# Performance work log

Measured on AMD Instinct MI355X. Metric: run time of the kernel, lower is better.

## Reference

```python
import jax, jax.numpy as jnp
import numpy as np

N_UP, N_DOWN, N_NUC, B = 16, 16, 8, 2048
EMB, TPS = 256, 32
N_ELEC = N_UP + N_DOWN


def mlp(x, w1, b1, w2, b2):
    # subnet: one hidden layer (tanh), linear output
    return jnp.tanh(x @ w1 + b1) @ w2 + b2


def _edge_indices():
    up = np.arange(N_UP)
    down = np.arange(N_UP, N_ELEC)

    def block_pairs(b):
        s, r = np.meshgrid(b, b, indexing='ij')
        m = s != r
        return s[m], r[m]

    s1, r1 = block_pairs(up)
    s2, r2 = block_pairs(down)
    senders_same = np.concatenate([s1, s2])
    receivers_same = np.concatenate([r1, r2])
    su, rd = np.meshgrid(up, down, indexing='ij')
    sd, ru = np.meshgrid(down, up, indexing='ij')
    senders_anti = np.concatenate([su.ravel(), sd.ravel()])
    receivers_anti = np.concatenate([rd.ravel(), ru.ravel()])
    senders_ne = np.repeat(np.arange(N_NUC), N_ELEC)
    receivers_ne = np.tile(np.arange(N_ELEC), N_NUC)
    return (senders_same, receivers_same, senders_anti, receivers_anti,
            senders_ne, receivers_ne)


def setup_inputs() -> dict:
    key = jax.random.key(0)
    ks = iter(jax.random.split(key, 32))

    def p(shape):
        return jax.random.normal(next(ks), shape, jnp.float32) * 0.1

    ss, rs, sa, ra, sn, rn = _edge_indices()
    inp = dict(
        electrons=p((B, N_ELEC, EMB)),
        nuclei=p((B, N_NUC, EMB)),
        feat_same=p((B, len(ss), TPS)),
        feat_anti=p((B, len(sa), TPS)),
        feat_ne=p((B, len(sn), TPS)),
        # u: per-edge-type deep-feature MLPs (TPS -> TPS)
        u_w1=p((3, TPS, TPS)), u_b1=jnp.zeros((3, TPS)),
        u_w2=p((3, TPS, TPS)), u_b2=jnp.zeros((3, TPS)),
        # w: per-edge-type message weight MLPs (TPS -> TPS)
        w_w1=p((3, TPS, TPS)), w_b1=jnp.zeros((3, TPS)),
        w_w2=p((3, TPS, TPS)), w_b2=jnp.zeros((3, TPS)),
        # h: per-edge-type sender-node MLPs (EMB -> TPS)
        h_w1=p((3, EMB, TPS)), h_b1=jnp.zeros((3, TPS)),
        h_w2=p((3, TPS, TPS)), h_b2=jnp.zeros((3, TPS)),
        # g: node update MLP (EMB + 3*TPS -> EMB), update_rule='concatenate'
        g_w1=p((EMB + 3 * TPS, EMB)), g_b1=jnp.zeros((EMB,)),
        g_w2=p((EMB, EMB)), g_b2=jnp.zeros((EMB,)),
        senders_same=jnp.asarray(ss, jnp.int32),
        receivers_same=jnp.asarray(rs, jnp.int32),
        senders_anti=jnp.asarray(sa, jnp.int32),
        receivers_anti=jnp.asarray(ra, jnp.int32),
        senders_ne=jnp.asarray(sn, jnp.int32),
        receivers_ne=jnp.asarray(rn, jnp.int32),
    )
    return inp


def reference(electrons, nuclei, feat_same, feat_anti, feat_ne,
              u_w1, u_b1, u_w2, u_b2,
              w_w1, w_b1, w_w2, w_b2,
              h_w1, h_b1, h_w2, h_b2,
              g_w1, g_b1, g_w2, g_b2,
              senders_same, receivers_same,
              senders_anti, receivers_anti,
              senders_ne, receivers_ne):
    feats = [feat_same, feat_anti, feat_ne]
    senders = [senders_same, senders_anti, senders_ne]
    receivers = [receivers_same, receivers_anti, receivers_ne]
    sender_nodes = [electrons, electrons, nuclei]
    z = []
    for t in range(3):  # fixed small set of edge types: same, anti, ne
        # deep features with two-particle residual (residual add)
        e = feats[t] + mlp(feats[t], u_w1[t], u_b1[t], u_w2[t], u_b2[t])
        we = mlp(e, w_w1[t], w_b1[t], w_w2[t], w_b2[t])              # [B, E_t, TPS]
        hx_nodes = mlp(sender_nodes[t], h_w1[t], h_b1[t], h_w2[t], h_b2[t])
        hx = hx_nodes[:, senders[t]]                                  # gather senders
        msg = we * hx
        # segment-sum over receivers into electron nodes
        zt = jnp.zeros((electrons.shape[0], N_ELEC, msg.shape[-1]), msg.dtype)
        z.append(zt.at[:, receivers[t]].add(msg))
    z_same, z_anti, z_ne = z
    # mean aggregation denominators (self_interaction=False -> self_mod=1)
    den_same = jnp.clip(jnp.concatenate(
        [jnp.full((N_UP, 1), N_UP - 1.0), jnp.full((N_DOWN, 1), N_DOWN - 1.0)]), 1.0)
    den_anti = jnp.clip(jnp.concatenate(
        [jnp.full((N_UP, 1), float(N_DOWN)), jnp.full((N_DOWN, 1), float(N_UP))]), 1.0)
    f = jnp.concatenate(
        [electrons, z_ne / N_NUC, z_same / den_same, z_anti / den_anti], axis=-1)
    updated = mlp(f, g_w1, g_b1, g_w2, g_b2)
    # one-particle residual (add)
    return electrons + updated
```

## Files before the change

### kernel.cpp

```cpp
#include <hip/hip_runtime.h>
#include <math.h>

#define NE 32
#define NN 8
#define EMB 256
#define TPS 32
#define E_SAME 480
#define E_ANTI 512
#define E_NE 256

#define AU1_OFF 0
#define AU2_OFF 3072
#define AW1_OFF 6144
#define AW2_OFF 9216
#define H1T_OFF 12288
#define H2T_OFF 36864
#define BIAS_OFF 39936
#define G1_OFF 40512
#define G2_OFF 130624

typedef float f32x4 __attribute__((ext_vector_type(4)));
typedef short s16x4 __attribute__((ext_vector_type(4)));
typedef short s16x8 __attribute__((ext_vector_type(8)));

__device__ __forceinline__ short f2bf(float x) {
    unsigned u = __builtin_bit_cast(unsigned, x);
    u += 0x7fffu + ((u >> 16) & 1u);
    return (short)(u >> 16);
}
__device__ __forceinline__ float bf2f(short h) {
    unsigned u = ((unsigned)(unsigned short)h) << 16;
    return __builtin_bit_cast(float, u);
}
__device__ __forceinline__ float fast_tanh(float x) {
    float e = __builtin_amdgcn_exp2f(x * 2.8853900817779268f);
    return 1.f - 2.f * __builtin_amdgcn_rcpf(e + 1.f);
}
__device__ __forceinline__ s16x8 pack8(float4 a, float4 b) {
    s16x8 r = { f2bf(a.x), f2bf(a.y), f2bf(a.z), f2bf(a.w),
                f2bf(b.x), f2bf(b.y), f2bf(b.z), f2bf(b.w) };
    return r;
}
__device__ __forceinline__ f32x4 mfma32(s16x8 a, s16x8 b, f32x4 c) {
    return __builtin_amdgcn_mfma_f32_16x16x32_bf16(a, b, c, 0, 0, 0);
}
__device__ __forceinline__ f32x4 mfma16(s16x4 a, s16x4 b, f32x4 c) {
#if __has_builtin(__builtin_amdgcn_mfma_f32_16x16x16bf16_1k)
    return __builtin_amdgcn_mfma_f32_16x16x16bf16_1k(a, b, c, 0, 0, 0);
#else
    asm volatile("v_mfma_f32_16x16x16_bf16 %0, %1, %2, %0" : "+v"(c) : "v"(a), "v"(b));
    return c;
#endif
}

__global__ void prep_weights(const float* __restrict__ u_w1, const float* __restrict__ u_w2,
                             const float* __restrict__ w_w1, const float* __restrict__ w_w2,
                             const float* __restrict__ h_w1, const float* __restrict__ h_w2,
                             const float* __restrict__ u_b1, const float* __restrict__ u_b2,
                             const float* __restrict__ w_b1, const float* __restrict__ w_b2,
                             const float* __restrict__ h_b1, const float* __restrict__ h_b2,
                             const float* __restrict__ g_w1, const float* __restrict__ g_w2,
                             short* __restrict__ wsb)
{
    int tile = blockIdx.x, lane = threadIdx.x;
    int g = lane >> 4, q = lane & 15;
    if (tile < 6) {
        int t = tile >> 1, mt = tile & 1;
        const float* src = u_w1 + t * 1024;
        short* dst = wsb + AU1_OFF + tile * 512 + lane * 8;
        #pragma unroll
        for (int i = 0; i < 8; ++i) dst[i] = f2bf(src[(8 * g + i) * 32 + mt * 16 + q]);
    } else if (tile < 42) {
        int m = (tile - 6) / 12, idx = (tile - 6) % 12;
        int mt = (idx >> 1) & 1, ks = idx & 1, t = idx >> 2;
        const float* mp = (m == 0) ? u_w2 : (m == 1) ? w_w1 : w_w2;
        const float* src = mp + t * 1024;
        short* dst = wsb + AU2_OFF + m * 3072 + idx * 256 + lane * 4;
        #pragma unroll
        for (int i = 0; i < 4; ++i) dst[i] = f2bf(src[(ks * 16 + 4 * g + i) * 32 + mt * 16 + q]);
    } else if (tile < 90) {
        int idx = tile - 42;
        int t = idx >> 4, r = idx & 15, mt = r >> 3, ks = r & 7;
        const float* src = h_w1 + t * 8192;
        short* dst = wsb + H1T_OFF + idx * 512 + lane * 8;
        #pragma unroll
        for (int i = 0; i < 8; ++i) dst[i] = f2bf(src[(ks * 32 + 8 * g + i) * 32 + mt * 16 + q]);
    } else if (tile < 102) {
        int idx = tile - 90;
        int t = idx >> 2, mt = (idx >> 1) & 1, ks = idx & 1;
        const float* src = h_w2 + t * 1024;
        short* dst = wsb + H2T_OFF + idx * 256 + lane * 4;
        #pragma unroll
        for (int i = 0; i < 4; ++i) dst[i] = f2bf(src[(ks * 16 + 4 * g + i) * 32 + mt * 16 + q]);
    } else if (tile == 102) {
        const float* bsrc[6] = {u_b1, u_b2, w_b1, w_b2, h_b1, h_b2};
        for (int j = lane; j < 576; j += 64)
            wsb[BIAS_OFF + j] = f2bf(bsrc[j / 96][j % 96]);
    } else if (tile < 279) {
        int idx = tile - 103, nt = idx / 11, ks = idx % 11;
        short* dst = wsb + G1_OFF + idx * 512 + lane * 8;
        #pragma unroll
        for (int i = 0; i < 8; ++i)
            dst[i] = f2bf(g_w1[(size_t)(ks * 32 + 8 * g + i) * 256 + nt * 16 + q]);
    } else {
        int idx = tile - 279;
        short* dst = wsb + G2_OFF + idx * 512 + lane * 8;
        int nt = idx >> 3, ks = idx & 7;
        #pragma unroll
        for (int i = 0; i < 8; ++i)
            dst[i] = f2bf(g_w2[(size_t)(ks * 32 + 8 * g + i) * 256 + nt * 16 + q]);
    }
}

__launch_bounds__(256, 4)
__global__ void gnn_kernel(
    const float* __restrict__ elec, const float* __restrict__ nuc,
    const float* __restrict__ fs,  const float* __restrict__ fa,  const float* __restrict__ fn,
    const float* __restrict__ g_b1, const float* __restrict__ g_b2,
    const int* __restrict__ ss, const int* __restrict__ rs,
    const int* __restrict__ sa, const int* __restrict__ ra,
    const int* __restrict__ sn, const int* __restrict__ rn,
    const short* __restrict__ wsb,
    float* __restrict__ out)
{
    __shared__ __align__(16) char smem[40384];
    short* f_s  = (short*)smem;
    float* z_s  = (float*)(smem + 22784);
    short* hx_s = (short*)(smem + 35200);
    short* H_s  = (short*)(smem + 22784);

    const int tid  = threadIdx.x;
    const int b    = blockIdx.x;
    const int lane = tid & 63, wv = tid >> 6;
    const int g    = lane >> 4, q = lane & 15;

    if (wv > 0)
        for (int i = tid - 64; i < 32 * 97; i += 192) z_s[i] = 0.f;

    #pragma unroll 1
    for (int task = wv; task < 5; task += 4) {
        int t, nt;
        if (task < 4) { t = task >> 1; nt = task & 1; }
        else          { t = 2; nt = 0; }
        const float* rowp = (t < 2) ? elec + ((size_t)b * NE + nt * 16 + q) * EMB
                                    : nuc  + ((size_t)b * NN + (q < 8 ? q : 7)) * EMB;
        f32x4 c0 = {0.f, 0.f, 0.f, 0.f}, c1 = {0.f, 0.f, 0.f, 0.f};
        const short* wA = wsb + H1T_OFF + t * 16 * 512;
        #pragma unroll
        for (int ks = 0; ks < 8; ++ks) {
            float4 v0 = *(const float4*)(rowp + 32 * ks + 8 * g);
            float4 v1 = *(const float4*)(rowp + 32 * ks + 8 * g + 4);
            s16x8 Bf = pack8(v0, v1);
            if (t == 0) {
                int off = (nt * 16 + q) * 356 + 32 * ks + 8 * g;
                *(s16x4*)(f_s + off)     = __builtin_shufflevector(Bf, Bf, 0, 1, 2, 3);
                *(s16x4*)(f_s + off + 4) = __builtin_shufflevector(Bf, Bf, 4, 5, 6, 7);
            }
            s16x8 a0 = *(const s16x8*)(wA + ks * 512 + lane * 8);
            s16x8 a1 = *(const s16x8*)(wA + (8 + ks) * 512 + lane * 8);
            c0 = mfma32(a0, Bf, c0);
            c1 = mfma32(a1, Bf, c1);
        }
        s16x4 b1l = *(const s16x4*)(wsb + BIAS_OFF + (12 + t) * 32 + 4 * g);
        s16x4 b1h = *(const s16x4*)(wsb + BIAS_OFF + (12 + t) * 32 + 16 + 4 * g);
        s16x4 p0, p1;
        #pragma unroll
        for (int r = 0; r < 4; ++r) {
            p0[r] = f2bf(fast_tanh(c0[r] + bf2f(b1l[r])));
            p1[r] = f2bf(fast_tanh(c1[r] + bf2f(b1h[r])));
        }
        const short* wA2 = wsb + H2T_OFF + t * 4 * 256;
        f32x4 d0 = {0.f, 0.f, 0.f, 0.f}, d1 = {0.f, 0.f, 0.f, 0.f};
        d0 = mfma16(*(const s16x4*)(wA2 + 0 * 256 + lane * 4), p0, d0);
        d0 = mfma16(*(const s16x4*)(wA2 + 1 * 256 + lane * 4), p1, d0);
        d1 = mfma16(*(const s16x4*)(wA2 + 2 * 256 + lane * 4), p0, d1);
        d1 = mfma16(*(const s16x4*)(wA2 + 3 * 256 + lane * 4), p1, d1);
        if (t < 2 || q < 8) {
            s16x4 b2l = *(const s16x4*)(wsb + BIAS_OFF + (15 + t) * 32 + 4 * g);
            s16x4 b2h = *(const s16x4*)(wsb + BIAS_OFF + (15 + t) * 32 + 16 + 4 * g);
            s16x4 w0, w1;
            #pragma unroll
            for (int r = 0; r < 4; ++r) {
                w0[r] = f2bf(d0[r] + bf2f(b2l[r]));
                w1[r] = f2bf(d1[r] + bf2f(b2h[r]));
            }
            int row = t * 32 + nt * 16 + q;
            *(s16x4*)(hx_s + row * 36 + 4 * g)      = w0;
            *(s16x4*)(hx_s + row * 36 + 16 + 4 * g) = w1;
        }
    }
    __syncthreads();

    #pragma unroll 1
    for (int t = 0; t < 3; ++t) {
        const float* ft; const int* snd; const int* rcv; int cnt, zc0;
        if (t == 0)      { ft = fs; snd = ss; rcv = rs; cnt = E_SAME; zc0 = 32; }
        else if (t == 1) { ft = fa; snd = sa; rcv = ra; cnt = E_ANTI; zc0 = 64; }
        else             { ft = fn; snd = sn; rcv = rn; cnt = E_NE;   zc0 = 0;  }
        s16x8 Au1_0 = *(const s16x8*)(wsb + AU1_OFF + (t * 2 + 0) * 512 + lane * 8);
        s16x8 Au1_1 = *(const s16x8*)(wsb + AU1_OFF + (t * 2 + 1) * 512 + lane * 8);
        s16x4 Au2_[4], Aw1_[4], Aw2_[4];
        #pragma unroll
        for (int i = 0; i < 4; ++i) {
            Au2_[i] = *(const s16x4*)(wsb + AU2_OFF + (t * 4 + i) * 256 + lane * 4);
            Aw1_[i] = *(const s16x4*)(wsb + AW1_OFF + (t * 4 + i) * 256 + lane * 4);
            Aw2_[i] = *(const s16x4*)(wsb + AW2_OFF + (t * 4 + i) * 256 + lane * 4);
        }
        s16x4 bb1l = *(const s16x4*)(wsb + BIAS_OFF + (0 + t) * 32 + 4 * g);
        s16x4 bb1h = *(const s16x4*)(wsb + BIAS_OFF + (0 + t) * 32 + 16 + 4 * g);
        s16x4 bb2l = *(const s16x4*)(wsb + BIAS_OFF + (3 + t) * 32 + 4 * g);
        s16x4 bb2h = *(const s16x4*)(wsb + BIAS_OFF + (3 + t) * 32 + 16 + 4 * g);
        s16x4 bb3l = *(const s16x4*)(wsb + BIAS_OFF + (6 + t) * 32 + 4 * g);
        s16x4 bb3h = *(const s16x4*)(wsb + BIAS_OFF + (6 + t) * 32 + 16 + 4 * g);
        s16x4 bb4l = *(const s16x4*)(wsb + BIAS_OFF + (9 + t) * 32 + 4 * g);
        s16x4 bb4h = *(const s16x4*)(wsb + BIAS_OFF + (9 + t) * 32 + 16 + 4 * g);
        const short* hxt = hx_s + t * 32 * 36;
        int ntile = cnt >> 4;

        const float* fp = ft + ((size_t)b * cnt + wv * 16 + q) * TPS;
        float4 v0 = *(const float4*)(fp + 8 * g);
        float4 v1 = *(const float4*)(fp + 8 * g + 4);
        float4 rl = *(const float4*)(fp + 4 * g);
        float4 rh = *(const float4*)(fp + 16 + 4 * g);
        int se = snd[wv * 16 + q], re = rcv[wv * 16 + q];

        #pragma unroll 1
        for (int tt = wv; tt < ntile; tt += 4) {
            int tn = tt + 4;
            float4 n0 = {0,0,0,0}, n1 = {0,0,0,0}, nrl = {0,0,0,0}, nrh = {0,0,0,0};
            int ns = 0, nr = 0;
            if (tn < ntile) {
                const float* np = ft + ((size_t)b * cnt + tn * 16 + q) * TPS;
                n0 = *(const float4*)(np + 8 * g);
                n1 = *(const float4*)(np + 8 * g + 4);
                nrl = *(const float4*)(np + 4 * g);
                nrh = *(const float4*)(np + 16 + 4 * g);
                ns = snd[tn * 16 + q]; nr = rcv[tn * 16 + q];
            }
            s16x8 B32 = pack8(v0, v1);
            f32x4 c0 = {0.f,0.f,0.f,0.f}, c1 = {0.f,0.f,0.f,0.f};
            c0 = mfma32(Au1_0, B32, c0);
            c1 = mfma32(Au1_1, B32, c1);
            s16x4 p0, p1;
            #pragma unroll
            for (int r = 0; r < 4; ++r) {
                p0[r] = f2bf(fast_tanh(c0[r] + bf2f(bb1l[r])));
                p1[r] = f2bf(fast_tanh(c1[r] + bf2f(bb1h[r])));
            }
            f32x4 d0 = {0.f,0.f,0.f,0.f}, d1 = {0.f,0.f,0.f,0.f};
            d0 = mfma16(Au2_[0], p0, d0); d0 = mfma16(Au2_[1], p1, d0);
            d1 = mfma16(Au2_[2], p0, d1); d1 = mfma16(Au2_[3], p1, d1);
            const float* rlp = (const float*)&rl; const float* rhp = (const float*)&rh;
            #pragma unroll
            for (int r = 0; r < 4; ++r) {
                p0[r] = f2bf(rlp[r] + d0[r] + bf2f(bb2l[r]));
                p1[r] = f2bf(rhp[r] + d1[r] + bf2f(bb2h[r]));
            }
            d0 = (f32x4){0.f,0.f,0.f,0.f}; d1 = (f32x4){0.f,0.f,0.f,0.f};
            d0 = mfma16(Aw1_[0], p0, d0); d0 = mfma16(Aw1_[1], p1, d0);
            d1 = mfma16(Aw1_[2], p0, d1); d1 = mfma16(Aw1_[3], p1, d1);
            #pragma unroll
            for (int r = 0; r < 4; ++r) {
                p0[r] = f2bf(fast_tanh(d0[r] + bf2f(bb3l[r])));
                p1[r] = f2bf(fast_tanh(d1[r] + bf2f(bb3h[r])));
            }
            d0 = (f32x4){0.f,0.f,0.f,0.f}; d1 = (f32x4){0.f,0.f,0.f,0.f};
            d0 = mfma16(Aw2_[0], p0, d0); d0 = mfma16(Aw2_[1], p1, d0);
            d1 = mfma16(Aw2_[2], p0, d1); d1 = mfma16(Aw2_[3], p1, d1);
            s16x4 hlo = *(const s16x4*)(hxt + se * 36 + 4 * g);
            s16x4 hhi = *(const s16x4*)(hxt + se * 36 + 16 + 4 * g);
            float* zr = z_s + re * 97 + zc0 + 4 * g;
            #pragma unroll
            for (int r = 0; r < 4; ++r) {
                atomicAdd(zr + r,      (d0[r] + bf2f(bb4l[r])) * bf2f(hlo[r]));
                atomicAdd(zr + 16 + r, (d1[r] + bf2f(bb4h[r])) * bf2f(hhi[r]));
            }
            v0 = n0; v1 = n1; rl = nrl; rh = nrh; se = ns; re = nr;
        }
    }
    __syncthreads();

    for (int i = tid; i < 32 * 96; i += 256) {
        int r = i / 96, c = i - r * 96;
        float sc = (c < 32) ? 0.125f : ((c < 64) ? (1.f / 15.f) : (1.f / 16.f));
        f_s[r * 356 + 256 + c] = f2bf(z_s[r * 97 + c] * sc);
    }
    __syncthreads();

    #pragma unroll 1
    for (int task = wv; task < 32; task += 4) {
        int mt = task >> 4, nt = task & 15;
        f32x4 acc = {0.f, 0.f, 0.f, 0.f};
        const short* ar = f_s + (mt * 16 + q) * 356 + 8 * g;
        const short* wp = wsb + G1_OFF + nt * 11 * 512 + lane * 8;
        #pragma unroll
        for (int ks = 0; ks < 11; ++ks) {
            s16x4 alo = *(const s16x4*)(ar + 32 * ks);
            s16x4 ahi = *(const s16x4*)(ar + 32 * ks + 4);
            s16x8 a = __builtin_shufflevector(alo, ahi, 0, 1, 2, 3, 4, 5, 6, 7);
            s16x8 bw = *(const s16x8*)(wp + ks * 512);
            acc = mfma32(a, bw, acc);
        }
        float bias = g_b1[nt * 16 + q];
        #pragma unroll
        for (int r = 0; r < 4; ++r)
            H_s[(mt * 16 + 4 * g + r) * 260 + nt * 16 + q] = f2bf(fast_tanh(acc[r] + bias));
    }
    __syncthreads();

    #pragma unroll 1
    for (int task = wv; task < 32; task += 4) {
        int mt = task >> 4, nt = task & 15;
        f32x4 acc = {0.f, 0.f, 0.f, 0.f};
        const short* ar = H_s + (mt * 16 + q) * 260 + 8 * g;
        const short* wp = wsb + G2_OFF + nt * 8 * 512 + lane * 8;
        #pragma unroll
        for (int ks = 0; ks < 8; ++ks) {
            s16x4 alo = *(const s16x4*)(ar + 32 * ks);
            s16x4 ahi = *(const s16x4*)(ar + 32 * ks + 4);
            s16x8 a = __builtin_shufflevector(alo, ahi, 0, 1, 2, 3, 4, 5, 6, 7);
            s16x8 bw = *(const s16x8*)(wp + ks * 512);
            acc = mfma32(a, bw, acc);
        }
        float bias = g_b2[nt * 16 + q];
        #pragma unroll
        for (int r = 0; r < 4; ++r) {
            int row = mt * 16 + 4 * g + r, col = nt * 16 + q;
            size_t o = ((size_t)b * NE + row) * EMB + col;
            out[o] = bf2f(f_s[row * 356 + col]) + acc[r] + bias;
        }
    }
}

extern "C" void kernel_launch(void* const* d_in, const int* in_sizes, int n_in,
                              void* d_out, int out_size, void* d_ws, size_t ws_size,
                              hipStream_t stream) {
    const float* elec = (const float*)d_in[0];
    const float* nuc  = (const float*)d_in[1];
    const float* fs   = (const float*)d_in[2];
    const float* fa   = (const float*)d_in[3];
    const float* fn   = (const float*)d_in[4];
    const float* u_w1 = (const float*)d_in[5];
    const float* u_b1 = (const float*)d_in[6];
    const float* u_w2 = (const float*)d_in[7];
    const float* u_b2 = (const float*)d_in[8];
    const float* w_w1 = (const float*)d_in[9];
    const float* w_b1 = (const float*)d_in[10];
    const float* w_w2 = (const float*)d_in[11];
    const float* w_b2 = (const float*)d_in[12];
    const float* h_w1 = (const float*)d_in[13];
    const float* h_b1 = (const float*)d_in[14];
    const float* h_w2 = (const float*)d_in[15];
    const float* h_b2 = (const float*)d_in[16];
    const float* g_w1 = (const float*)d_in[17];
    const float* g_b1 = (const float*)d_in[18];
    const float* g_w2 = (const float*)d_in[19];
    const float* g_b2 = (const float*)d_in[20];
    const int* ss = (const int*)d_in[21];
    const int* rs = (const int*)d_in[22];
    const int* sa = (const int*)d_in[23];
    const int* ra = (const int*)d_in[24];
    const int* sn = (const int*)d_in[25];
    const int* rn = (const int*)d_in[26];

    short* wsb = (short*)d_ws;
    int nb = in_sizes[0] / (NE * EMB);

    prep_weights<<<407, 64, 0, stream>>>(u_w1, u_w2, w_w1, w_w2, h_w1, h_w2,
                                         u_b1, u_b2, w_b1, w_b2, h_b1, h_b2,
                                         g_w1, g_w2, wsb);
    gnn_kernel<<<nb, 256, 0, stream>>>(elec, nuc, fs, fa, fn, g_b1, g_b2,
                                       ss, rs, sa, ra, sn, rn, wsb, (float*)d_out);
}
```

Baseline: 473.6 us.

## Split fused GNN kernel into hx, edge and update kernels via global scratch

Breaks the single per-batch kernel into three launches. One computes sender-node h-MLP outputs for all batches into global memory, one runs the edge MLPs and scatter-add and writes scaled bf16 aggregates to global memory, and one reloads the electrons and aggregates to run the node-update MLP. The aim is to cut per-kernel shared memory and register pressure and to spread the small h-MLP work across all waves instead of leaving three of four waves idle. The cost is extra global round-trips for hx and z, an extra reload of the electrons, and two more kernel launches.

```diff
diff --git a/kernel.cpp b/kernel.cpp
--- a/kernel.cpp
+++ b/kernel.cpp
@@ -18,6 +18,8 @@
 #define BIAS_OFF 39936
 #define G1_OFF 40512
 #define G2_OFF 130624
+#define HX_OFF  196608
+#define ZS_OFF  4915200
 
 typedef float f32x4 __attribute__((ext_vector_type(4)));
 typedef short s16x4 __attribute__((ext_vector_type(4)));
@@ -39,6 +41,11 @@
 __device__ __forceinline__ s16x8 pack8(float4 a, float4 b) {
     s16x8 r = { f2bf(a.x), f2bf(a.y), f2bf(a.z), f2bf(a.w),
                 f2bf(b.x), f2bf(b.y), f2bf(b.z), f2bf(b.w) };
+    return r;
+}
+__device__ __forceinline__ s16x8 pack8v(f32x4 a, f32x4 b) {
+    s16x8 r = { f2bf(a[0]), f2bf(a[1]), f2bf(a[2]), f2bf(a[3]),
+                f2bf(b[0]), f2bf(b[1]), f2bf(b[2]), f2bf(b[3]) };
     return r;
 }
 __device__ __forceinline__ f32x4 mfma32(s16x8 a, s16x8 b, f32x4 c) {
@@ -113,82 +120,77 @@
 }
 
 __launch_bounds__(256, 4)
-__global__ void gnn_kernel(
-    const float* __restrict__ elec, const float* __restrict__ nuc,
+__global__ void hx_kernel(const float* __restrict__ elec, const float* __restrict__ nuc,
+                          const short* __restrict__ wsb, short* __restrict__ hxg)
+{
+    const int lane = threadIdx.x & 63, wv = threadIdx.x >> 6;
+    const int g = lane >> 4, q = lane & 15;
+    const int wave_gid = blockIdx.x * 4 + wv;
+    const int b = wave_gid / 5, task = wave_gid % 5;
+
+    int t, nt;
+    if (task < 4) { t = task >> 1; nt = task & 1; }
+    else          { t = 2; nt = 0; }
+    const float* rowp = (t < 2) ? elec + ((size_t)b * NE + nt * 16 + q) * EMB
+                                : nuc  + ((size_t)b * NN + (q < 8 ? q : 7)) * EMB;
+    f32x4 c0 = {0.f, 0.f, 0.f, 0.f}, c1 = {0.f, 0.f, 0.f, 0.f};
+    const short* wA = wsb + H1T_OFF + t * 16 * 512;
+    #pragma unroll
+    for (int ks = 0; ks < 8; ++ks) {
+        float4 v0 = *(const float4*)(rowp + 32 * ks + 8 * g);
+        float4 v1 = *(const float4*)(rowp + 32 * ks + 8 * g + 4);
+        s16x8 Bf = pack8(v0, v1);
+        s16x8 a0 = *(const s16x8*)(wA + ks * 512 + lane * 8);
+        s16x8 a1 = *(const s16x8*)(wA + (8 + ks) * 512 + lane * 8);
+        c0 = mfma32(a0, Bf, c0);
+        c1 = mfma32(a1, Bf, c1);
+    }
+    s16x4 b1l = *(const s16x4*)(wsb + BIAS_OFF + (12 + t) * 32 + 4 * g);
+    s16x4 b1h = *(const s16x4*)(wsb + BIAS_OFF + (12 + t) * 32 + 16 + 4 * g);
+    s16x4 p0, p1;
+    #pragma unroll
+    for (int r = 0; r < 4; ++r) {
+        p0[r] = f2bf(fast_tanh(c0[r] + bf2f(b1l[r])));
+        p1[r] = f2bf(fast_tanh(c1[r] + bf2f(b1h[r])));
+    }
+    const short* wA2 = wsb + H2T_OFF + t * 4 * 256;
+    f32x4 d0 = {0.f, 0.f, 0.f, 0.f}, d1 = {0.f, 0.f, 0.f, 0.f};
+    d0 = mfma16(*(const s16x4*)(wA2 + 0 * 256 + lane * 4), p0, d0);
+    d0 = mfma16(*(const s16x4*)(wA2 + 1 * 256 + lane * 4), p1, d0);
+    d1 = mfma16(*(const s16x4*)(wA2 + 2 * 256 + lane * 4), p0, d1);
+    d1 = mfma16(*(const s16x4*)(wA2 + 3 * 256 + lane * 4), p1, d1);
+    if (t < 2 || q < 8) {
+        s16x4 b2l = *(const s16x4*)(wsb + BIAS_OFF + (15 + t) * 32 + 4 * g);
+        s16x4 b2h = *(const s16x4*)(wsb + BIAS_OFF + (15 + t) * 32 + 16 + 4 * g);
+        s16x4 w0, w1;
+        #pragma unroll
+        for (int r = 0; r < 4; ++r) {
+            w0[r] = f2bf(d0[r] + bf2f(b2l[r]));
+            w1[r] = f2bf(d1[r] + bf2f(b2h[r]));
+        }
+        int row = t * 32 + nt * 16 + q;
+        short* dst = hxg + ((size_t)b * 72 + row) * 32;
+        *(s16x4*)(dst + 4 * g)      = w0;
+        *(s16x4*)(dst + 16 + 4 * g) = w1;
+    }
+}
+
+__launch_bounds__(256, 4)
+__global__ void edge_kernel(
     const float* __restrict__ fs,  const float* __restrict__ fa,  const float* __restrict__ fn,
-    const float* __restrict__ g_b1, const float* __restrict__ g_b2,
     const int* __restrict__ ss, const int* __restrict__ rs,
     const int* __restrict__ sa, const int* __restrict__ ra,
     const int* __restrict__ sn, const int* __restrict__ rn,
-    const short* __restrict__ wsb,
-    float* __restrict__ out)
+    const short* __restrict__ wsb, const short* __restrict__ hxg,
+    short* __restrict__ zsg)
 {
-    __shared__ __align__(16) char smem[40384];
-    short* f_s  = (short*)smem;
-    float* z_s  = (float*)(smem + 22784);
-    short* hx_s = (short*)(smem + 35200);
-    short* H_s  = (short*)(smem + 22784);
-
+    __shared__ __align__(16) float z_s[32 * 97];
     const int tid  = threadIdx.x;
     const int b    = blockIdx.x;
     const int lane = tid & 63, wv = tid >> 6;
     const int g    = lane >> 4, q = lane & 15;
 
-    if (wv > 0)
-        for (int i = tid - 64; i < 32 * 97; i += 192) z_s[i] = 0.f;
-
-    #pragma unroll 1
-    for (int task = wv; task < 5; task += 4) {
-        int t, nt;
-        if (task < 4) { t = task >> 1; nt = task & 1; }
-        else          { t = 2; nt = 0; }
-        const float* rowp = (t < 2) ? elec + ((size_t)b * NE + nt * 16 + q) * EMB
-                                    : nuc  + ((size_t)b * NN + (q < 8 ? q : 7)) * EMB;
-        f32x4 c0 = {0.f, 0.f, 0.f, 0.f}, c1 = {0.f, 0.f, 0.f, 0.f};
-        const short* wA = wsb + H1T_OFF + t * 16 * 512;
-        #pragma unroll
-        for (int ks = 0; ks < 8; ++ks) {
-            float4 v0 = *(const float4*)(rowp + 32 * ks + 8 * g);
-            float4 v1 = *(const float4*)(rowp + 32 * ks + 8 * g + 4);
-            s16x8 Bf = pack8(v0, v1);
-            if (t == 0) {
-                int off = (nt * 16 + q) * 356 + 32 * ks + 8 * g;
-                *(s16x4*)(f_s + off)     = __builtin_shufflevector(Bf, Bf, 0, 1, 2, 3);
-                *(s16x4*)(f_s + off + 4) = __builtin_shufflevector(Bf, Bf, 4, 5, 6, 7);
-            }
-            s16x8 a0 = *(const s16x8*)(wA + ks * 512 + lane * 8);
-            s16x8 a1 = *(const s16x8*)(wA + (8 + ks) * 512 + lane * 8);
-            c0 = mfma32(a0, Bf, c0);
-            c1 = mfma32(a1, Bf, c1);
-        }
-        s16x4 b1l = *(const s16x4*)(wsb + BIAS_OFF + (12 + t) * 32 + 4 * g);
-        s16x4 b1h = *(const s16x4*)(wsb + BIAS_OFF + (12 + t) * 32 + 16 + 4 * g);
-        s16x4 p0, p1;
-        #pragma unroll
-        for (int r = 0; r < 4; ++r) {
-            p0[r] = f2bf(fast_tanh(c0[r] + bf2f(b1l[r])));
-            p1[r] = f2bf(fast_tanh(c1[r] + bf2f(b1h[r])));
-        }
-        const short* wA2 = wsb + H2T_OFF + t * 4 * 256;
-        f32x4 d0 = {0.f, 0.f, 0.f, 0.f}, d1 = {0.f, 0.f, 0.f, 0.f};
-        d0 = mfma16(*(const s16x4*)(wA2 + 0 * 256 + lane * 4), p0, d0);
-        d0 = mfma16(*(const s16x4*)(wA2 + 1 * 256 + lane * 4), p1, d0);
-        d1 = mfma16(*(const s16x4*)(wA2 + 2 * 256 + lane * 4), p0, d1);
-        d1 = mfma16(*(const s16x4*)(wA2 + 3 * 256 + lane * 4), p1, d1);
-        if (t < 2 || q < 8) {
-            s16x4 b2l = *(const s16x4*)(wsb + BIAS_OFF + (15 + t) * 32 + 4 * g);
-            s16x4 b2h = *(const s16x4*)(wsb + BIAS_OFF + (15 + t) * 32 + 16 + 4 * g);
-            s16x4 w0, w1;
-            #pragma unroll
-            for (int r = 0; r < 4; ++r) {
-                w0[r] = f2bf(d0[r] + bf2f(b2l[r]));
-                w1[r] = f2bf(d1[r] + bf2f(b2h[r]));
-            }
-            int row = t * 32 + nt * 16 + q;
-            *(s16x4*)(hx_s + row * 36 + 4 * g)      = w0;
-            *(s16x4*)(hx_s + row * 36 + 16 + 4 * g) = w1;
-        }
-    }
+    for (int i = tid; i < 32 * 97; i += 256) z_s[i] = 0.f;
     __syncthreads();
 
     #pragma unroll 1
@@ -214,7 +216,7 @@
         s16x4 bb3h = *(const s16x4*)(wsb + BIAS_OFF + (6 + t) * 32 + 16 + 4 * g);
         s16x4 bb4l = *(const s16x4*)(wsb + BIAS_OFF + (9 + t) * 32 + 4 * g);
         s16x4 bb4h = *(const s16x4*)(wsb + BIAS_OFF + (9 + t) * 32 + 16 + 4 * g);
-        const short* hxt = hx_s + t * 32 * 36;
+        const short* hxt = hxg + ((size_t)b * 72 + t * 32) * 32;
         int ntile = cnt >> 4;
 
         const float* fp = ft + ((size_t)b * cnt + wv * 16 + q) * TPS;
@@ -267,8 +269,8 @@
             d0 = (f32x4){0.f,0.f,0.f,0.f}; d1 = (f32x4){0.f,0.f,0.f,0.f};
             d0 = mfma16(Aw2_[0], p0, d0); d0 = mfma16(Aw2_[1], p1, d0);
             d1 = mfma16(Aw2_[2], p0, d1); d1 = mfma16(Aw2_[3], p1, d1);
-            s16x4 hlo = *(const s16x4*)(hxt + se * 36 + 4 * g);
-            s16x4 hhi = *(const s16x4*)(hxt + se * 36 + 16 + 4 * g);
+            s16x4 hlo = *(const s16x4*)(hxt + se * 32 + 4 * g);
+            s16x4 hhi = *(const s16x4*)(hxt + se * 32 + 16 + 4 * g);
             float* zr = z_s + re * 97 + zc0 + 4 * g;
             #pragma unroll
             for (int r = 0; r < 4; ++r) {
@@ -280,10 +282,47 @@
     }
     __syncthreads();
 
-    for (int i = tid; i < 32 * 96; i += 256) {
-        int r = i / 96, c = i - r * 96;
-        float sc = (c < 32) ? 0.125f : ((c < 64) ? (1.f / 15.f) : (1.f / 16.f));
-        f_s[r * 356 + 256 + c] = f2bf(z_s[r * 97 + c] * sc);
+    for (int u = tid; u < 384; u += 256) {
+        int r = u / 12, c8 = u - r * 12;
+        float sc = (c8 < 4) ? 0.125f : ((c8 < 8) ? (1.f / 15.f) : (1.f / 16.f));
+        const float* zp = z_s + r * 97 + c8 * 8;
+        s16x8 v;
+        #pragma unroll
+        for (int j = 0; j < 8; ++j) v[j] = f2bf(zp[j] * sc);
+        *(s16x8*)(zsg + (size_t)b * 3072 + r * 96 + c8 * 8) = v;
+    }
+}
+
+__launch_bounds__(256, 4)
+__global__ void upd_kernel(const float* __restrict__ elec,
+                           const float* __restrict__ g_b1, const float* __restrict__ g_b2,
+                           const short* __restrict__ wsb, const short* __restrict__ zsg,
+                           float* __restrict__ out)
+{
+    __shared__ __align__(16) char smem[39424];
+    short* f_s = (short*)smem;
+    short* H_s = (short*)(smem + 22784);
+
+    const int tid  = threadIdx.x;
+    const int b    = blockIdx.x;
+    const int lane = tid & 63, wv = tid >> 6;
+    const int g    = lane >> 4, q = lane & 15;
+
+    {
+        int row = tid >> 3, ch = tid & 7;
+        const float* src = elec + ((size_t)b * NE + row) * EMB + ch * 32;
+        short* dst = f_s + row * 356 + ch * 32;
+        #pragma unroll
+        for (int i = 0; i < 4; ++i) {
+            float4 v0 = *(const float4*)(src + 8 * i);
+            float4 v1 = *(const float4*)(src + 8 * i + 4);
+            *(s16x8*)(dst + 8 * i) = pack8(v0, v1);
+        }
+    }
+    for (int u = tid; u < 384; u += 256) {
+        int r = u / 12, c8 = u - r * 12;
+        *(s16x8*)(f_s + r * 356 + 256 + c8 * 8) =
+            *(const s16x8*)(zsg + (size_t)b * 3072 + r * 96 + c8 * 8);
     }
     __syncthreads();
 
@@ -364,11 +403,15 @@
     const int* rn = (const int*)d_in[26];
 
     short* wsb = (short*)d_ws;
+    short* hxg = wsb + HX_OFF;
+    short* zsg = wsb + ZS_OFF;
     int nb = in_sizes[0] / (NE * EMB);
 
     prep_weights<<<407, 64, 0, stream>>>(u_w1, u_w2, w_w1, w_w2, h_w1, h_w2,
                                          u_b1, u_b2, w_b1, w_b2, h_b1, h_b2,
                                          g_w1, g_w2, wsb);
-    gnn_kernel<<<nb, 256, 0, stream>>>(elec, nuc, fs, fa, fn, g_b1, g_b2,
-                                       ss, rs, sa, ra, sn, rn, wsb, (float*)d_out);
-}
+    hx_kernel<<<(nb * 5 + 3) / 4, 256, 0, stream>>>(elec, nuc, wsb, hxg);
+    edge_kernel<<<nb, 256, 0, stream>>>(fs, fa, fn, ss, rs, sa, ra, sn, rn,
+                                        wsb, hxg, zsg);
+    upd_kernel<<<nb, 256, 0, stream>>>(elec, g_b1, g_b2, wsb, zsg, (float*)d_out);
+}
```

After: 516.9 us. 9.1% more time.
